# Kernel tuning notes

Measured on AMD Instinct MI355X. Metric: run time of the kernel, lower is better.

Reference implementation:

```python
import jax, jax.numpy as jnp
import numpy as np
from itertools import combinations

B, M = 128, 24
EMB = 16
NEG_SLOPE = 0.01  # torch F.leaky_relu default


def _combo_index():
    # 60 combinations: choose 2 of 4 hole cards x choose 3 of 5 board cards.
    hero = list(combinations(range(4), 2))      # 6
    board = list(combinations(range(5), 3))     # 10
    combos = []
    for h in hero:
        for b in board:
            combos.append([h[0], h[1], 4 + b[0], 4 + b[1], 4 + b[2]])
    return np.asarray(combos, dtype=np.int32)   # (60, 5)

_COMBOS = jnp.asarray(_combo_index())


def setup_inputs() -> dict:
    key = jax.random.key(0)
    ks = jax.random.split(key, 12)
    ranks = jax.random.randint(ks[0], (B, M, 9), 1, 14)   # 1..13
    suits = jax.random.randint(ks[1], (B, M, 9), 1, 5)    # 1..4
    x = jnp.stack([ranks, suits], axis=-1).reshape(B, M, 18).astype(jnp.int64)

    def lin(k, fan_in, fan_out):
        bound = 1.0 / np.sqrt(fan_in)
        kw, kb = jax.random.split(k)
        W = jax.random.uniform(kw, (fan_in, fan_out), minval=-bound, maxval=bound, dtype=jnp.float32)
        b = jax.random.uniform(kb, (fan_out,), minval=-bound, maxval=bound, dtype=jnp.float32)
        return W, b

    card_emb = jax.random.normal(ks[2], (53, EMB), dtype=jnp.float32)
    card_emb = card_emb.at[0].set(0.0)  # padding_idx=0
    hand_W, hand_b = lin(ks[3], 32, 128)
    board_W, board_b = lin(ks[4], 48, 128)
    hidden_W, hidden_b = lin(ks[5], 256, 256)
    out_W, out_b = lin(ks[6], 60 * 256, 256)
    return {"x": x, "card_emb": card_emb,
            "hand_W": hand_W, "hand_b": hand_b,
            "board_W": board_W, "board_b": board_b,
            "hidden_W": hidden_W, "hidden_b": hidden_b,
            "out_W": out_W, "out_b": out_b}


def reference(x, card_emb, hand_W, hand_b, board_W, board_b,
              hidden_W, hidden_b, out_W, out_b):
    act = lambda v: jax.nn.leaky_relu(v, NEG_SLOPE)
    Bx, Mx = x.shape[0], x.shape[1]
    ranks = x[..., 0::2]                       # (B,M,9)
    suits = x[..., 1::2]
    rc = jnp.take(ranks, _COMBOS, axis=-1)     # (B,M,60,5)
    sc = jnp.take(suits, _COMBOS, axis=-1)
    rc = jnp.where(rc > 0, rc - 1, 0)          # ranks -> 0..12
    sc = jnp.where(sc > 0, (sc - 1) * 13, 0)   # suit offset 0/13/26/39
    cards = rc + sc                            # (B,M,60,5) in [0,52)
    emb = card_emb[cards]                      # (B,M,60,5,16)
    hero = emb[..., :2, :].reshape(Bx, Mx, 60, 32)
    board = emb[..., 2:, :].reshape(Bx, Mx, 60, 48)
    hero = act(hero @ hand_W + hand_b)         # (B,M,60,128)
    board = act(board @ board_W + board_b)     # (B,M,60,128)
    h = act(jnp.concatenate([hero, board], axis=-1) @ hidden_W + hidden_b)  # (B,M,60,256)
    flat = h.reshape(Bx, Mx, 60 * 256)         # (B,M,15360)
    return act(flat @ out_W + out_b)           # (B,M,256)
```

## Files before the change

kernel.cpp:

```cpp
#include <hip/hip_runtime.h>
#include <hip/hip_bf16.h>
#include <cstdint>
#include <cstddef>

typedef __hip_bfloat16 bf16;
typedef __attribute__((ext_vector_type(8))) short short8;
typedef __attribute__((ext_vector_type(4))) float floatx4;

#define KO 15360
#define KS 16
#define KSLICE 960
#define NIT (KSLICE / 64)

__device__ __forceinline__ float lrelu(float v) { return v > 0.f ? v : 0.01f * v; }

__device__ __forceinline__ float bflo(unsigned int u) {
  unsigned int x = u << 16; float f; __builtin_memcpy(&f, &x, 4); return f;
}
__device__ __forceinline__ float bfhi(unsigned int u) {
  unsigned int x = u & 0xffff0000u; float f; __builtin_memcpy(&f, &x, 4); return f;
}
__device__ __forceinline__ unsigned int pk2(float lo, float hi) {
  bf16 a = __float2bfloat16(lo), b = __float2bfloat16(hi);
  unsigned short ua, ub;
  __builtin_memcpy(&ua, &a, 2); __builtin_memcpy(&ub, &b, 2);
  return (unsigned int)ua | ((unsigned int)ub << 16);
}
__device__ __forceinline__ unsigned int hpair(unsigned int u, unsigned int v) {
  return pk2(lrelu(bflo(u) + bflo(v)), lrelu(bfhi(u) + bfhi(v)));
}

__device__ __forceinline__ void async_lds16(const bf16* g, bf16* l) {
  __builtin_amdgcn_global_load_lds((__attribute__((address_space(1))) void*)(g),
                                   (__attribute__((address_space(3))) void*)(l),
                                   16, 0, 0);
}

__global__ __launch_bounds__(256) void prep(
    const float* __restrict__ hidden_W, bf16* __restrict__ hWtp,
    const float* __restrict__ out_W, bf16* __restrict__ oWt)
{
  __shared__ float sbuf[64 * 65];
  const int t = threadIdx.x;
  const int id = blockIdx.x;

  if (id < 16) {
    const int g = id;
    float* Lt = sbuf;
    for (int i = t; i < 4096; i += 256)
      Lt[i] = hidden_W[(size_t)(i >> 4) * 256 + g * 16 + (i & 15)];
    __syncthreads();
    #pragma unroll
    for (int cc = 0; cc < 2; ++cc) {
      int c = t + 256 * cc;
      int ks = c >> 6, l = c & 63, lr = l & 15, quad = l >> 4;
      short8 v;
      #pragma unroll
      for (int j = 0; j < 8; ++j) {
        bf16 b = __float2bfloat16(Lt[(ks * 32 + quad * 8 + j) * 16 + lr]);
        short s; __builtin_memcpy(&s, &b, 2);
        v[j] = s;
      }
      *(short8*)(hWtp + ((size_t)(g * 8 + ks) * 64 + l) * 8) = v;
    }
  } else {
    const int id2 = id - 16;
    const int kb = (id2 % 240) * 64;
    const int nb = (id2 / 240) * 64;
    float (*tile)[65] = (float(*)[65])sbuf;
    #pragma unroll
    for (int i = 0; i < 16; ++i) {
      int idx = t + 256 * i;
      int r = idx >> 6, c = idx & 63;
      tile[r][c] = out_W[(size_t)(kb + r) * 256 + nb + c];
    }
    __syncthreads();
    #pragma unroll
    for (int i = 0; i < 16; ++i) {
      int idx = t + 256 * i;
      int r = idx >> 6, c = idx & 63;
      oWt[(size_t)(nb + r) * KO + kb + c] = __float2bfloat16(tile[c][r]);
    }
  }
}

__global__ __launch_bounds__(256, 2) void hb_uv(
    const int* __restrict__ x, const float* __restrict__ card_emb,
    const float* __restrict__ hand_W, const float* __restrict__ hand_b,
    const float* __restrict__ board_W, const float* __restrict__ board_b,
    const bf16* __restrict__ hWtp, const float* __restrict__ hidden_b,
    bf16* __restrict__ UV)
{
  static constexpr int H0[6] = {0,0,0,1,1,2};
  static constexpr int H1[6] = {1,2,3,2,3,3};
  static constexpr int B0[10] = {0,0,0,0,0,0,1,1,1,2};
  static constexpr int B1[10] = {1,1,1,2,2,3,2,2,3,3};
  static constexpr int B2[10] = {2,3,4,3,4,4,3,4,4,4};

  __shared__ float wH[32 * 128];
  __shared__ float wB[48 * 128];
  __shared__ float bH[128], bB[128];
  __shared__ float emb[6][9][16];
  __shared__ bf16 At[2][16][264];

  const int t = threadIdx.x;
  const int w = t >> 6, l = t & 63, lr = l & 15, quad = l >> 4;
  const int item0 = blockIdx.x * 6;

  for (int i = t * 4; i < 4096; i += 1024) *(float4*)&wH[i] = *(const float4*)&hand_W[i];
  for (int i = t * 4; i < 6144; i += 1024) *(float4*)&wB[i] = *(const float4*)&board_W[i];
  if (t < 128) { bH[t] = hand_b[t]; bB[t] = board_b[t]; }
  for (int ii = t; ii < 864; ii += 256) {
    int li = ii / 144, idx = ii - li * 144;
    int ci = idx >> 4, e = idx & 15;
    int rk = x[(item0 + li) * 18 + 2 * ci], st = x[(item0 + li) * 18 + 2 * ci + 1];
    int card = (rk > 0 ? rk - 1 : 0) + (st > 0 ? (st - 1) * 13 : 0);
    emb[li][ci][e] = card_emb[card * 16 + e];
  }
  __syncthreads();

  short8 bfrag[4][8];
  float bias[4];
  #pragma unroll
  for (int tl = 0; tl < 4; ++tl) {
    bias[tl] = hidden_b[w * 64 + tl * 16 + lr];
    #pragma unroll
    for (int ks = 0; ks < 8; ++ks)
      bfrag[tl][ks] = *(const short8*)(hWtp + ((size_t)((w * 4 + tl) * 8 + ks) * 64 + l) * 8);
  }

  const int half = t >> 7, j = t & 127;

  for (int pass = 0; pass < 3; ++pass) {
    if (pass) __syncthreads();
    const int embi = 2 * pass + half;
    {
      bf16 z = __float2bfloat16(0.f);
      #pragma unroll
      for (int p = 0; p < 6; ++p) At[half][p][128 + j] = z;
      #pragma unroll
      for (int b = 0; b < 10; ++b) At[half][6 + b][j] = z;
    }
    float aH[6], aB[10];
    {
      float hb = bH[j], bb = bB[j];
      #pragma unroll
      for (int p = 0; p < 6; ++p) aH[p] = hb;
      #pragma unroll
      for (int b = 0; b < 10; ++b) aB[b] = bb;
    }
    #pragma unroll
    for (int k = 0; k < 16; ++k) {
      float e[9];
      #pragma unroll
      for (int c = 0; c < 9; ++c) e[c] = emb[embi][c][k];
      float w0 = wH[k * 128 + j], w1 = wH[(16 + k) * 128 + j];
      float v0 = wB[k * 128 + j], v1 = wB[(16 + k) * 128 + j], v2 = wB[(32 + k) * 128 + j];
      #pragma unroll
      for (int p = 0; p < 6; ++p)
        aH[p] += e[H0[p]] * w0 + e[H1[p]] * w1;
      #pragma unroll
      for (int b = 0; b < 10; ++b)
        aB[b] += e[4 + B0[b]] * v0 + e[4 + B1[b]] * v1 + e[4 + B2[b]] * v2;
    }
    #pragma unroll
    for (int p = 0; p < 6; ++p) At[half][p][j] = __float2bfloat16(lrelu(aH[p]));
    #pragma unroll
    for (int b = 0; b < 10; ++b) At[half][6 + b][128 + j] = __float2bfloat16(lrelu(aB[b]));
    __syncthreads();

    #pragma unroll
    for (int li = 0; li < 2; ++li) {
      short8 a[8];
      #pragma unroll
      for (int ks = 0; ks < 8; ++ks)
        a[ks] = *(const short8*)&At[li][lr][ks * 32 + quad * 8];

      floatx4 acc[4];
      floatx4 zero = {0.f, 0.f, 0.f, 0.f};
      #pragma unroll
      for (int i = 0; i < 4; ++i) acc[i] = zero;
      #pragma unroll
      for (int ks = 0; ks < 8; ++ks)
        #pragma unroll
        for (int tl = 0; tl < 4; ++tl)
          acc[tl] = __builtin_amdgcn_mfma_f32_16x16x32_bf16(a[ks], bfrag[tl][ks], acc[tl], 0, 0, 0);

      bf16* dst = UV + (size_t)(item0 + 2 * pass + li) * 4096;
      #pragma unroll
      for (int tl = 0; tl < 4; ++tl) {
        int n = w * 64 + tl * 16 + lr;
        #pragma unroll
        for (int r = 0; r < 4; ++r) {
          int m = quad * 4 + r;
          float v = acc[tl][r] + (m >= 6 ? bias[tl] : 0.f);
          dst[m * 256 + n] = __float2bfloat16(v);
        }
      }
    }
  }
}

__device__ __forceinline__ void uv_fetch(const bf16* __restrict__ UV, int m0, int ar,
                                         int ac, int ks0, int it,
                                         uint4& u0, uint4& u1, uint4& v0, uint4& v1)
{
  const int gk = ks0 + it * 64;
  const int combo = gk >> 8;
  const int urow = combo / 10, vrow = 6 + (combo - urow * 10);
  const int c0 = gk & 255;
  const bf16* ub = UV + ((size_t)(m0 + ar) * 16 + urow) * 256 + c0 + ac * 16;
  const bf16* vb = UV + ((size_t)(m0 + ar) * 16 + vrow) * 256 + c0 + ac * 16;
  u0 = *(const uint4*)ub;  u1 = *(const uint4*)(ub + 8);
  v0 = *(const uint4*)vb;  v1 = *(const uint4*)(vb + 8);
}

__global__ __launch_bounds__(256, 2) void out_gemm(
    const bf16* __restrict__ UV, const bf16* __restrict__ Wt,
    float* __restrict__ pbuf)
{
  __shared__ bf16 As[64 * 64];
  __shared__ bf16 Bs[256 * 64];

  const int t = threadIdx.x;
  const int id = blockIdx.x;
  const int by = ((id & 7) << 1) | ((id >> 3) & 1);
  const int bx = id >> 4;
  const int w = t >> 6, l = t & 63, lr = l & 15, quad = l >> 4;
  const int m0 = bx * 64;
  const int ks0 = by * KSLICE;
  const int ar = t >> 2, ac = t & 3;

  const bf16* rowp[8];
  {
    int rl = l >> 3, j = (l & 7) ^ rl;
    #pragma unroll
    for (int q = 0; q < 8; ++q)
      rowp[q] = Wt + (size_t)(w * 64 + 8 * q + rl) * KO + ks0 + j * 8;
  }
  bf16* BsW = &Bs[w * 4096];

  floatx4 acc[16];
  floatx4 zero = {0.f, 0.f, 0.f, 0.f};
  #pragma unroll
  for (int i = 0; i < 16; ++i) acc[i] = zero;

  uint4 cu0, cu1, cv0, cv1;
  uv_fetch(UV, m0, ar, ac, ks0, 0, cu0, cu1, cv0, cv1);

  for (int it = 0; it < NIT; ++it) {
    __syncthreads();

    #pragma unroll
    for (int q = 0; q < 8; ++q)
      async_lds16(rowp[q] + it * 64, BsW + q * 512);

    {
      uint4 h0, h1;
      h0.x = hpair(cu0.x, cv0.x); h0.y = hpair(cu0.y, cv0.y);
      h0.z = hpair(cu0.z, cv0.z); h0.w = hpair(cu0.w, cv0.w);
      h1.x = hpair(cu1.x, cv1.x); h1.y = hpair(cu1.y, cv1.y);
      h1.z = hpair(cu1.z, cv1.z); h1.w = hpair(cu1.w, cv1.w);
      int jA0 = (2 * ac) ^ (ar & 7);
      int jA1 = (2 * ac + 1) ^ (ar & 7);
      *(uint4*)&As[ar * 64 + jA0 * 8] = h0;
      *(uint4*)&As[ar * 64 + jA1 * 8] = h1;
    }

    __syncthreads();

    if (it + 1 < NIT)
      uv_fetch(UV, m0, ar, ac, ks0, it + 1, cu0, cu1, cv0, cv1);

    #pragma unroll
    for (int ks = 0; ks < 2; ++ks) {
      short8 af[4], bfr[4];
      #pragma unroll
      for (int i = 0; i < 4; ++i) {
        int row = i * 16 + lr;
        int jp = (4 * ks + quad) ^ (row & 7);
        af[i] = *(const short8*)&As[row * 64 + jp * 8];
      }
      #pragma unroll
      for (int j = 0; j < 4; ++j) {
        int row = w * 64 + j * 16 + lr;
        int jp = (4 * ks + quad) ^ (row & 7);
        bfr[j] = *(const short8*)&Bs[row * 64 + jp * 8];
      }
      #pragma unroll
      for (int i = 0; i < 4; ++i)
        #pragma unroll
        for (int j = 0; j < 4; ++j)
          acc[i * 4 + j] = __builtin_amdgcn_mfma_f32_16x16x32_bf16(af[i], bfr[j], acc[i * 4 + j], 0, 0, 0);
    }
  }

  float* dst = pbuf + (((size_t)by * 48 + bx) * 4 + w) * 4096 + l;
  #pragma unroll
  for (int a = 0; a < 16; ++a)
    #pragma unroll
    for (int r = 0; r < 4; ++r)
      dst[(a * 4 + r) * 64] = acc[a][r];
}

__global__ __launch_bounds__(256) void reduce_bias(
    const float* __restrict__ pbuf, const float* __restrict__ outb,
    float* __restrict__ out, int slice_stride)
{
  int i4 = blockIdx.x * 256 + threadIdx.x;
  int idx = i4 * 4;
  float4 s = *(const float4*)&pbuf[idx];
  #pragma unroll
  for (int k = 1; k < KS; ++k) {
    float4 v = *(const float4*)&pbuf[idx + (size_t)k * slice_stride];
    s.x += v.x; s.y += v.y; s.z += v.z; s.w += v.w;
  }
  int l = idx & 63, q = (idx >> 6) & 63, w2 = (idx >> 12) & 3, bx = idx >> 14;
  int a = q >> 2, r = q & 3, i = a >> 2, tl = a & 3;
  int lr = l & 15, quad = l >> 4;
  int m = bx * 64 + i * 16 + quad * 4 + r;
  int n = w2 * 64 + tl * 16 + lr;
  float4 b = *(const float4*)&outb[n];
  float4 rr;
  rr.x = lrelu(s.x + b.x); rr.y = lrelu(s.y + b.y);
  rr.z = lrelu(s.z + b.z); rr.w = lrelu(s.w + b.w);
  *(float4*)&out[(size_t)m * 256 + n] = rr;
}

extern "C" void kernel_launch(void* const* d_in, const int* in_sizes, int n_in,
                              void* d_out, int out_size, void* d_ws, size_t ws_size,
                              hipStream_t stream)
{
  const int*   x        = (const int*)  d_in[0];
  const float* card_emb = (const float*)d_in[1];
  const float* hand_W   = (const float*)d_in[2];
  const float* hand_b   = (const float*)d_in[3];
  const float* board_W  = (const float*)d_in[4];
  const float* board_b  = (const float*)d_in[5];
  const float* hidden_W = (const float*)d_in[6];
  const float* hidden_b = (const float*)d_in[7];
  const float* out_W    = (const float*)d_in[8];
  const float* out_b    = (const float*)d_in[9];
  float* out = (float*)d_out;

  const int NI = in_sizes[0] / 18;

  char* ws = (char*)d_ws;
  bf16* hWtp = (bf16*)ws;
  bf16* oWt  = (bf16*)(ws + 131072);
  bf16* UV   = (bf16*)(ws + 131072 + 7864320);
  float* pbuf = (float*)(ws + 131072 + 7864320 + (size_t)NI * 8192);

  prep<<<16 + 240 * 4, 256, 0, stream>>>(hidden_W, hWtp, out_W, oWt);
  hb_uv<<<NI / 6, 256, 0, stream>>>(x, card_emb, hand_W, hand_b,
                                    board_W, board_b, hWtp, hidden_b, UV);
  out_gemm<<<NI / 64 * KS, 256, 0, stream>>>(UV, oWt, pbuf);
  reduce_bias<<<NI / 4, 256, 0, stream>>>(pbuf, out_b, out, NI * 256);
}
```

Measured before the change: 185.0 us.

## Split hand/board embedding stage from hidden-layer MFMA GEMM into separate kernels

```diff
diff --git a/kernel.cpp b/kernel.cpp
--- a/kernel.cpp
+++ b/kernel.cpp
@@ -11,6 +11,7 @@
 #define KS 16
 #define KSLICE 960
 #define NIT (KSLICE / 64)
+#define IPB 12
 
 __device__ __forceinline__ float lrelu(float v) { return v > 0.f ? v : 0.01f * v; }
 
@@ -84,12 +85,11 @@
   }
 }
 
-__global__ __launch_bounds__(256, 2) void hb_uv(
+__global__ __launch_bounds__(256) void hb_pack(
     const int* __restrict__ x, const float* __restrict__ card_emb,
     const float* __restrict__ hand_W, const float* __restrict__ hand_b,
     const float* __restrict__ board_W, const float* __restrict__ board_b,
-    const bf16* __restrict__ hWtp, const float* __restrict__ hidden_b,
-    bf16* __restrict__ UV)
+    bf16* __restrict__ Abuf)
 {
   static constexpr int H0[6] = {0,0,0,1,1,2};
   static constexpr int H1[6] = {1,2,3,2,3,3};
@@ -100,17 +100,16 @@
   __shared__ float wH[32 * 128];
   __shared__ float wB[48 * 128];
   __shared__ float bH[128], bB[128];
-  __shared__ float emb[6][9][16];
+  __shared__ float emb[4][9][16];
   __shared__ bf16 At[2][16][264];
 
   const int t = threadIdx.x;
-  const int w = t >> 6, l = t & 63, lr = l & 15, quad = l >> 4;
-  const int item0 = blockIdx.x * 6;
+  const int item0 = blockIdx.x * 4;
 
   for (int i = t * 4; i < 4096; i += 1024) *(float4*)&wH[i] = *(const float4*)&hand_W[i];
   for (int i = t * 4; i < 6144; i += 1024) *(float4*)&wB[i] = *(const float4*)&board_W[i];
   if (t < 128) { bH[t] = hand_b[t]; bB[t] = board_b[t]; }
-  for (int ii = t; ii < 864; ii += 256) {
+  for (int ii = t; ii < 576; ii += 256) {
     int li = ii / 144, idx = ii - li * 144;
     int ci = idx >> 4, e = idx & 15;
     int rk = x[(item0 + li) * 18 + 2 * ci], st = x[(item0 + li) * 18 + 2 * ci + 1];
@@ -119,19 +118,9 @@
   }
   __syncthreads();
 
-  short8 bfrag[4][8];
-  float bias[4];
-  #pragma unroll
-  for (int tl = 0; tl < 4; ++tl) {
-    bias[tl] = hidden_b[w * 64 + tl * 16 + lr];
-    #pragma unroll
-    for (int ks = 0; ks < 8; ++ks)
-      bfrag[tl][ks] = *(const short8*)(hWtp + ((size_t)((w * 4 + tl) * 8 + ks) * 64 + l) * 8);
-  }
-
   const int half = t >> 7, j = t & 127;
 
-  for (int pass = 0; pass < 3; ++pass) {
+  for (int pass = 0; pass < 2; ++pass) {
     if (pass) __syncthreads();
     const int embi = 2 * pass + half;
     {
@@ -170,30 +159,77 @@
     __syncthreads();
 
     #pragma unroll
+    for (int li2 = 0; li2 < 2; ++li2) {
+      #pragma unroll
+      for (int cc = 0; cc < 2; ++cc) {
+        int c = t + 256 * cc;
+        int m = c & 15, kq = (c >> 4) & 3, ks = c >> 6;
+        short8 v = *(const short8*)&At[li2][m][ks * 32 + kq * 8];
+        *(short8*)(Abuf + (size_t)(item0 + 2 * pass + li2) * 4096 + (size_t)c * 8) = v;
+      }
+    }
+    __syncthreads();
+  }
+}
+
+__global__ __launch_bounds__(256, 2) void uv_gemm(
+    const bf16* __restrict__ Abuf, const bf16* __restrict__ hWtp,
+    const float* __restrict__ hidden_b, bf16* __restrict__ UV)
+{
+  __shared__ bf16 hL[32768];
+
+  const int t = threadIdx.x, w = t >> 6, l = t & 63;
+  const int lr = l & 15, quad = l >> 4;
+  const int half = blockIdx.y;
+  const int item0 = blockIdx.x * IPB;
+
+  const bf16* src = hWtp + (size_t)half * 32768;
+  #pragma unroll
+  for (int i = 0; i < 16; ++i)
+    async_lds16(src + (size_t)(i * 256 + t) * 8, hL + (size_t)(i * 256 + t) * 8);
+
+  float bias[2];
+  #pragma unroll
+  for (int tl = 0; tl < 2; ++tl)
+    bias[tl] = hidden_b[half * 128 + (w * 2 + tl) * 16 + lr];
+
+  __syncthreads();
+
+  for (int ip = 0; ip < IPB / 2; ++ip) {
+    const bf16* abA = Abuf + (size_t)(item0 + 2 * ip) * 4096;
+    const bf16* abB = abA + 4096;
+    short8 aA[8], aB[8];
+    #pragma unroll
+    for (int ks = 0; ks < 8; ++ks) {
+      aA[ks] = *(const short8*)(abA + (size_t)(ks * 64 + l) * 8);
+      aB[ks] = *(const short8*)(abB + (size_t)(ks * 64 + l) * 8);
+    }
+
+    floatx4 accA[2], accB[2];
+    floatx4 zero = {0.f, 0.f, 0.f, 0.f};
+    #pragma unroll
+    for (int i = 0; i < 2; ++i) { accA[i] = zero; accB[i] = zero; }
+
+    #pragma unroll
+    for (int tl = 0; tl < 2; ++tl)
+      #pragma unroll
+      for (int ks = 0; ks < 8; ++ks) {
+        short8 bfr = *(const short8*)&hL[(size_t)(((w * 2 + tl) * 8 + ks) * 64 + l) * 8];
+        accA[tl] = __builtin_amdgcn_mfma_f32_16x16x32_bf16(aA[ks], bfr, accA[tl], 0, 0, 0);
+        accB[tl] = __builtin_amdgcn_mfma_f32_16x16x32_bf16(aB[ks], bfr, accB[tl], 0, 0, 0);
+      }
+
+    #pragma unroll
     for (int li = 0; li < 2; ++li) {
-      short8 a[8];
-      #pragma unroll
-      for (int ks = 0; ks < 8; ++ks)
-        a[ks] = *(const short8*)&At[li][lr][ks * 32 + quad * 8];
-
-      floatx4 acc[4];
-      floatx4 zero = {0.f, 0.f, 0.f, 0.f};
-      #pragma unroll
-      for (int i = 0; i < 4; ++i) acc[i] = zero;
-      #pragma unroll
-      for (int ks = 0; ks < 8; ++ks)
-        #pragma unroll
-        for (int tl = 0; tl < 4; ++tl)
-          acc[tl] = __builtin_amdgcn_mfma_f32_16x16x32_bf16(a[ks], bfrag[tl][ks], acc[tl], 0, 0, 0);
-
-      bf16* dst = UV + (size_t)(item0 + 2 * pass + li) * 4096;
-      #pragma unroll
-      for (int tl = 0; tl < 4; ++tl) {
-        int n = w * 64 + tl * 16 + lr;
+      bf16* dst = UV + (size_t)(item0 + 2 * ip + li) * 4096;
+      #pragma unroll
+      for (int tl = 0; tl < 2; ++tl) {
+        int n = half * 128 + (w * 2 + tl) * 16 + lr;
+        floatx4 acc = li ? accB[tl] : accA[tl];
         #pragma unroll
         for (int r = 0; r < 4; ++r) {
           int m = quad * 4 + r;
-          float v = acc[tl][r] + (m >= 6 ? bias[tl] : 0.f);
+          float v = acc[r] + (m >= 6 ? bias[tl] : 0.f);
           dst[m * 256 + n] = __float2bfloat16(v);
         }
       }
@@ -349,11 +385,13 @@
   bf16* hWtp = (bf16*)ws;
   bf16* oWt  = (bf16*)(ws + 131072);
   bf16* UV   = (bf16*)(ws + 131072 + 7864320);
-  float* pbuf = (float*)(ws + 131072 + 7864320 + (size_t)NI * 8192);
+  bf16* Abuf = (bf16*)(ws + 131072 + 7864320 + (size_t)NI * 8192);
+  float* pbuf = (float*)Abuf;
 
   prep<<<16 + 240 * 4, 256, 0, stream>>>(hidden_W, hWtp, out_W, oWt);
-  hb_uv<<<NI / 6, 256, 0, stream>>>(x, card_emb, hand_W, hand_b,
-                                    board_W, board_b, hWtp, hidden_b, UV);
+  hb_pack<<<NI / 4, 256, 0, stream>>>(x, card_emb, hand_W, hand_b,
+                                      board_W, board_b, Abuf);
+  uv_gemm<<<dim3(NI / IPB, 2), 256, 0, stream>>>(Abuf, hWtp, hidden_b, UV);
   out_gemm<<<NI / 64 * KS, 256, 0, stream>>>(UV, oWt, pbuf);
   reduce_bias<<<NI / 4, 256, 0, stream>>>(pbuf, out_b, out, NI * 256);
 }
```

Result: faster. 168.1 us (-9.2%).

## Stage hidden_W fragments through LDS instead of registers and give each wave its own item

Applied to the files above, without the earlier changes.

```diff
diff --git a/kernel.cpp b/kernel.cpp
--- a/kernel.cpp
+++ b/kernel.cpp
@@ -97,20 +97,24 @@
   static constexpr int B1[10] = {1,1,1,2,2,3,2,2,3,3};
   static constexpr int B2[10] = {2,3,4,3,4,4,3,4,4,4};
 
-  __shared__ float wH[32 * 128];
-  __shared__ float wB[48 * 128];
-  __shared__ float bH[128], bB[128];
-  __shared__ float emb[6][9][16];
-  __shared__ bf16 At[2][16][264];
+  __shared__ __align__(16) char uni[40960];
+  __shared__ float bH[128], bB[128], biasH[256];
+  __shared__ float emb[4][9][16];
+  __shared__ bf16 At[4][16][264];
+
+  float* wH = (float*)uni;
+  float* wB = (float*)(uni + 16384);
+  bf16*  hQ = (bf16*)uni;
 
   const int t = threadIdx.x;
   const int w = t >> 6, l = t & 63, lr = l & 15, quad = l >> 4;
-  const int item0 = blockIdx.x * 6;
+  const int item0 = blockIdx.x * 4;
 
   for (int i = t * 4; i < 4096; i += 1024) *(float4*)&wH[i] = *(const float4*)&hand_W[i];
   for (int i = t * 4; i < 6144; i += 1024) *(float4*)&wB[i] = *(const float4*)&board_W[i];
   if (t < 128) { bH[t] = hand_b[t]; bB[t] = board_b[t]; }
-  for (int ii = t; ii < 864; ii += 256) {
+  biasH[t] = hidden_b[t];
+  for (int ii = t; ii < 576; ii += 256) {
     int li = ii / 144, idx = ii - li * 144;
     int ci = idx >> 4, e = idx & 15;
     int rk = x[(item0 + li) * 18 + 2 * ci], st = x[(item0 + li) * 18 + 2 * ci + 1];
@@ -119,27 +123,16 @@
   }
   __syncthreads();
 
-  short8 bfrag[4][8];
-  float bias[4];
-  #pragma unroll
-  for (int tl = 0; tl < 4; ++tl) {
-    bias[tl] = hidden_b[w * 64 + tl * 16 + lr];
-    #pragma unroll
-    for (int ks = 0; ks < 8; ++ks)
-      bfrag[tl][ks] = *(const short8*)(hWtp + ((size_t)((w * 4 + tl) * 8 + ks) * 64 + l) * 8);
-  }
-
   const int half = t >> 7, j = t & 127;
-
-  for (int pass = 0; pass < 3; ++pass) {
-    if (pass) __syncthreads();
-    const int embi = 2 * pass + half;
+  #pragma unroll
+  for (int pass = 0; pass < 2; ++pass) {
+    const int li = 2 * pass + half;
     {
       bf16 z = __float2bfloat16(0.f);
       #pragma unroll
-      for (int p = 0; p < 6; ++p) At[half][p][128 + j] = z;
-      #pragma unroll
-      for (int b = 0; b < 10; ++b) At[half][6 + b][j] = z;
+      for (int p = 0; p < 6; ++p) At[li][p][128 + j] = z;
+      #pragma unroll
+      for (int b = 0; b < 10; ++b) At[li][6 + b][j] = z;
     }
     float aH[6], aB[10];
     {
@@ -153,7 +146,7 @@
     for (int k = 0; k < 16; ++k) {
       float e[9];
       #pragma unroll
-      for (int c = 0; c < 9; ++c) e[c] = emb[embi][c][k];
+      for (int c = 0; c < 9; ++c) e[c] = emb[li][c][k];
       float w0 = wH[k * 128 + j], w1 = wH[(16 + k) * 128 + j];
       float v0 = wB[k * 128 + j], v1 = wB[(16 + k) * 128 + j], v2 = wB[(32 + k) * 128 + j];
       #pragma unroll
@@ -164,38 +157,41 @@
         aB[b] += e[4 + B0[b]] * v0 + e[4 + B1[b]] * v1 + e[4 + B2[b]] * v2;
     }
     #pragma unroll
-    for (int p = 0; p < 6; ++p) At[half][p][j] = __float2bfloat16(lrelu(aH[p]));
-    #pragma unroll
-    for (int b = 0; b < 10; ++b) At[half][6 + b][128 + j] = __float2bfloat16(lrelu(aB[b]));
-    __syncthreads();
-
-    #pragma unroll
-    for (int li = 0; li < 2; ++li) {
-      short8 a[8];
-      #pragma unroll
-      for (int ks = 0; ks < 8; ++ks)
-        a[ks] = *(const short8*)&At[li][lr][ks * 32 + quad * 8];
-
-      floatx4 acc[4];
-      floatx4 zero = {0.f, 0.f, 0.f, 0.f};
-      #pragma unroll
-      for (int i = 0; i < 4; ++i) acc[i] = zero;
-      #pragma unroll
-      for (int ks = 0; ks < 8; ++ks)
-        #pragma unroll
-        for (int tl = 0; tl < 4; ++tl)
-          acc[tl] = __builtin_amdgcn_mfma_f32_16x16x32_bf16(a[ks], bfrag[tl][ks], acc[tl], 0, 0, 0);
-
-      bf16* dst = UV + (size_t)(item0 + 2 * pass + li) * 4096;
-      #pragma unroll
-      for (int tl = 0; tl < 4; ++tl) {
-        int n = w * 64 + tl * 16 + lr;
-        #pragma unroll
-        for (int r = 0; r < 4; ++r) {
-          int m = quad * 4 + r;
-          float v = acc[tl][r] + (m >= 6 ? bias[tl] : 0.f);
-          dst[m * 256 + n] = __float2bfloat16(v);
-        }
+    for (int p = 0; p < 6; ++p) At[li][p][j] = __float2bfloat16(lrelu(aH[p]));
+    #pragma unroll
+    for (int b = 0; b < 10; ++b) At[li][6 + b][128 + j] = __float2bfloat16(lrelu(aB[b]));
+  }
+  __syncthreads();
+
+  short8 a[8];
+  #pragma unroll
+  for (int ks = 0; ks < 8; ++ks)
+    a[ks] = *(const short8*)&At[w][lr][ks * 32 + quad * 8];
+
+  bf16* dst = UV + (size_t)(item0 + w) * 4096;
+
+  for (int q = 0; q < 4; ++q) {
+    if (q) __syncthreads();
+    #pragma unroll
+    for (int i = 0; i < 8; ++i)
+      async_lds16(hWtp + (size_t)q * 16384 + (size_t)(i * 256 + t) * 8,
+                  hQ + (size_t)(i * 256 + t) * 8);
+    __syncthreads();
+
+    #pragma unroll
+    for (int tl = 0; tl < 4; ++tl) {
+      floatx4 acc = {0.f, 0.f, 0.f, 0.f};
+      #pragma unroll
+      for (int ks = 0; ks < 8; ++ks) {
+        short8 bfr = *(const short8*)&hQ[(size_t)((tl * 8 + ks) * 64 + l) * 8];
+        acc = __builtin_amdgcn_mfma_f32_16x16x32_bf16(a[ks], bfr, acc, 0, 0, 0);
+      }
+      int n = q * 64 + tl * 16 + lr;
+      float bn = biasH[n];
+      #pragma unroll
+      for (int r = 0; r < 4; ++r) {
+        int m = quad * 4 + r;
+        dst[m * 256 + n] = __float2bfloat16(acc[r] + (m >= 6 ? bn : 0.f));
       }
     }
   }
@@ -352,7 +348,7 @@
   float* pbuf = (float*)(ws + 131072 + 7864320 + (size_t)NI * 8192);
 
   prep<<<16 + 240 * 4, 256, 0, stream>>>(hidden_W, hWtp, out_W, oWt);
-  hb_uv<<<NI / 6, 256, 0, stream>>>(x, card_emb, hand_W, hand_b,
+  hb_uv<<<NI / 4, 256, 0, stream>>>(x, card_emb, hand_W, hand_b,
                                     board_W, board_b, hWtp, hidden_b, UV);
   out_gemm<<<NI / 64 * KS, 256, 0, stream>>>(UV, oWt, pbuf);
   reduce_bias<<<NI / 4, 256, 0, stream>>>(pbuf, out_b, out, NI * 256);
```

After: 197.3 us. +6.7%, slower.
